# Kernel tuning notes

Measured on AMD Instinct MI355X. Metric: run time of the kernel, lower is better.

## Reference

```python
import jax, jax.numpy as jnp
import numpy as np

N, D_IN, D_OUT, L, R = 32768, 2048, 2048, 8, 16
LORA_ALPHA, LORA_RANK = 32.0, 16.0
SCALE = LORA_ALPHA / LORA_RANK  # applied because alpha != rank


def setup_inputs() -> dict:
    key = jax.random.key(0)
    ks = jax.random.split(key, 6)
    x = jax.random.normal(ks[0], (N, D_IN), dtype=jnp.float32)
    W = jax.random.normal(ks[1], (D_OUT, D_IN), dtype=jnp.float32) * 0.02
    b = jax.random.normal(ks[2], (D_OUT,), dtype=jnp.float32) * 0.02
    A_all = jax.random.normal(ks[3], (L, R, D_IN), dtype=jnp.float32) * 0.02
    B_all = jax.random.normal(ks[4], (L, D_OUT, R), dtype=jnp.float32) * 0.02
    # per-sample adapter index; -1 would mean "no LoRA" (handled by mask below)
    lora_idx = jax.random.randint(ks[5], (N,), 0, L, dtype=jnp.int32)
    return {"x": x, "W": W, "b": b, "A_all": A_all, "B_all": B_all, "lora_idx": lora_idx}


def reference(x, W, b, A_all, B_all, lora_idx):
    # Base linear: base_layer(x) -> x @ W.T + b
    base_out = x @ W.T + b  # [N, D_OUT]
    # Multi-LoRA: per-token adapter selection. Instead of Python grouping
    # (gather-matmul-scatter per group), compute the tiny down-projection for
    # all adapters and mask-select, then one fused up-projection.
    u = jnp.einsum('nd,lrd->nlr', x, A_all)  # [N, L, R] (small: r=16)
    Lnum = A_all.shape[0]
    sel = (lora_idx[:, None] == jnp.arange(Lnum, dtype=lora_idx.dtype)[None, :]) \
          & (lora_idx >= 0)[:, None]  # [N, L] one-hot, zero row if idx < 0
    u = u * sel[:, :, None].astype(u.dtype) * jnp.asarray(SCALE, u.dtype)
    # delta[n] = scale * (x[n] @ A[idx_n].T) @ B[idx_n].T, zeros elsewhere
    delta = jnp.einsum('nlr,lor->no', u, B_all)  # [N, D_OUT]
    return base_out + delta
```

## Files before the change

### kernel.cpp

```cpp
#include <hip/hip_runtime.h>
#include <stdint.h>

#define N_TOK 32768
#define DIN   2048
#define DOUT  2048
#define LAD   8
#define RRK   16
#define KCAT  2176
#define SCALE 2.0f

typedef __attribute__((ext_vector_type(8))) short bf16x8;
typedef __attribute__((ext_vector_type(4))) float f32x4;

__device__ __forceinline__ unsigned short f2bf(float f) {
    union { float f; unsigned u; } c; c.f = f;
    return (unsigned short)((c.u + 0x7FFFu + ((c.u >> 16) & 1u)) >> 16);
}

__device__ __forceinline__ uint4 pack8(float4 a, float4 b) {
    union { unsigned short s[8]; uint4 v; } u;
    u.s[0] = f2bf(a.x); u.s[1] = f2bf(a.y); u.s[2] = f2bf(a.z); u.s[3] = f2bf(a.w);
    u.s[4] = f2bf(b.x); u.s[5] = f2bf(b.y); u.s[6] = f2bf(b.z); u.s[7] = f2bf(b.w);
    return u.v;
}

__device__ __forceinline__ void async16(const void* g, void* l) {
    __builtin_amdgcn_global_load_lds(
        (const __attribute__((address_space(1))) void*)g,
        (__attribute__((address_space(3))) void*)l, 16, 0, 0);
}

__global__ __launch_bounds__(256) void prep_w(const float* __restrict__ W,
                                              const float* __restrict__ A_all,
                                              const float* __restrict__ B_all,
                                              unsigned short* __restrict__ wcat,
                                              unsigned short* __restrict__ acat) {
    const int NW = DOUT * DIN / 8;
    const int NB = DOUT * LAD;
    const int NA = LAD * RRK * DIN / 8;
    int tid = blockIdx.x * 256 + threadIdx.x;
    if (tid < NW) {
        int e = tid * 8;
        int o = e / DIN, k = e % DIN;
        float4 f0 = *(const float4*)(W + e);
        float4 f1 = *(const float4*)(W + e + 4);
        *(uint4*)(wcat + (size_t)o * KCAT + k) = pack8(f0, f1);
    } else if (tid < NW + NB) {
        int t = tid - NW;
        int o = t >> 3, l = t & 7;
        const float* src = B_all + ((size_t)l * DOUT + o) * RRK;
        float4 f0 = *(const float4*)(src + 0);
        float4 f1 = *(const float4*)(src + 4);
        float4 f2 = *(const float4*)(src + 8);
        float4 f3 = *(const float4*)(src + 12);
        unsigned short* dst = wcat + (size_t)o * KCAT + DIN + l * RRK;
        *(uint4*)(dst + 0) = pack8(f0, f1);
        *(uint4*)(dst + 8) = pack8(f2, f3);
    } else if (tid < NW + NB + NA) {
        int e = (tid - NW - NB) * 8;
        float4 f0 = *(const float4*)(A_all + e);
        float4 f1 = *(const float4*)(A_all + e + 4);
        *(uint4*)(acat + e) = pack8(f0, f1);
    }
}

__global__ __launch_bounds__(256) void conv_x(const float* __restrict__ x,
                                              unsigned short* __restrict__ xcat) {
    size_t e = ((size_t)blockIdx.x * 256 + threadIdx.x) * 8;
    int n = (int)(e / DIN), k = (int)(e % DIN);
    float4 f0 = *(const float4*)(x + e);
    float4 f1 = *(const float4*)(x + e + 4);
    *(uint4*)(xcat + (size_t)n * KCAT + k) = pack8(f0, f1);
}

__global__ __launch_bounds__(256) void u_gemm(const unsigned short* __restrict__ xcat,
                                              const unsigned short* __restrict__ acat,
                                              const int* __restrict__ lidx,
                                              unsigned short* __restrict__ xcat_w) {
    __shared__ short As[128 * 32];
    __shared__ short Bs[128 * 32];
    const int tid = threadIdx.x;
    const int lane = tid & 63, wv = tid >> 6;
    const int wm = wv >> 1, wn = wv & 1;
    const int quad = lane >> 4, lm = lane & 15;
    const int row0 = blockIdx.x * 128;
    const int sg = (lane & 3) ^ ((lane >> 3) & 3);
    const int swg = quad ^ ((lm >> 1) & 3);

    f32x4 acc[4][4];
    f32x4 zero = {0.f, 0.f, 0.f, 0.f};
#pragma unroll
    for (int i = 0; i < 4; ++i)
#pragma unroll
        for (int j = 0; j < 4; ++j) acc[i][j] = zero;

    for (int kt = 0; kt < DIN / 32; ++kt) {
        const unsigned short* ga = xcat + (size_t)row0 * KCAT + kt * 32;
        const unsigned short* gb = acat + kt * 32;
        __syncthreads();
#pragma unroll
        for (int it = 0; it < 2; ++it) {
            int cw = it * 4 + wv;
            int r = (cw * 64 + lane) >> 2;
            async16(ga + (size_t)r * KCAT + sg * 8, (void*)(As + cw * 512));
            async16(gb + (size_t)r * DIN + sg * 8, (void*)(Bs + cw * 512));
        }
        __syncthreads();
        bf16x8 a[4], b[4];
#pragma unroll
        for (int mi = 0; mi < 4; ++mi)
            a[mi] = *(const bf16x8*)&As[(wm * 64 + mi * 16 + lm) * 32 + swg * 8];
#pragma unroll
        for (int ni = 0; ni < 4; ++ni)
            b[ni] = *(const bf16x8*)&Bs[(wn * 64 + ni * 16 + lm) * 32 + swg * 8];
#pragma unroll
        for (int mi = 0; mi < 4; ++mi)
#pragma unroll
            for (int ni = 0; ni < 4; ++ni)
                acc[mi][ni] = __builtin_amdgcn_mfma_f32_16x16x32_bf16(a[mi], b[ni], acc[mi][ni], 0, 0, 0);
    }

#pragma unroll
    for (int mi = 0; mi < 4; ++mi) {
#pragma unroll
        for (int e = 0; e < 4; ++e) {
            int t = row0 + wm * 64 + mi * 16 + quad * 4 + e;
            int l = lidx[t];
#pragma unroll
            for (int ni = 0; ni < 4; ++ni) {
                int j = wn * 64 + ni * 16 + lm;
                float v = ((j >> 4) == l) ? acc[mi][ni][e] * SCALE : 0.0f;
                xcat_w[(size_t)t * KCAT + DIN + j] = f2bf(v);
            }
        }
    }
}

#define BK2  64
#define NKT2 (KCAT / BK2)
#define NIT  (NKT2 / 2)

#define VMC4() asm volatile("s_waitcnt vmcnt(4)" ::: "memory")
#define VMC0() asm volatile("s_waitcnt vmcnt(0)" ::: "memory")
#define LGK8() asm volatile("s_waitcnt lgkmcnt(8)" ::: "memory")
#define LGK0() asm volatile("s_waitcnt lgkmcnt(0)" ::: "memory")
#define BARR() __builtin_amdgcn_s_barrier()
#define SBR()  __builtin_amdgcn_sched_barrier(0)
#define PRIO1() __builtin_amdgcn_s_setprio(1)
#define PRIO0() __builtin_amdgcn_s_setprio(0)

#define RD_A(D, QM)                                                            \
    _Pragma("unroll") for (int mi = 0; mi < 4; ++mi)                           \
    _Pragma("unroll") for (int ks = 0; ks < 2; ++ks) {                         \
        const int rl = ((QM) * 4 + mi) * 16 + lm;                              \
        const int ob = (rl * 128 + ks * 64 + quad * 16) ^ ((lm & 7) << 4);     \
        aF[mi * 2 + ks] = *(const bf16x8*)((const char*)&lds[D][wm][0] + ob);  \
    }

#define RD_B(D, QN, BF)                                                        \
    _Pragma("unroll") for (int ni = 0; ni < 2; ++ni)                           \
    _Pragma("unroll") for (int ks = 0; ks < 2; ++ks) {                         \
        const int rl = (wn & 1) * 64 + ((QN) * 2 + ni) * 16 + lm;              \
        const int ob = (rl * 128 + ks * 64 + quad * 16) ^ ((lm & 7) << 4);     \
        BF[ni * 2 + ks] =                                                      \
            *(const bf16x8*)((const char*)&lds[D][2 + (wn >> 1)][0] + ob);     \
    }

#define MFMA16(QM, QN, BF)                                                     \
    _Pragma("unroll") for (int mi = 0; mi < 4; ++mi)                           \
    _Pragma("unroll") for (int ni = 0; ni < 2; ++ni)                           \
    _Pragma("unroll") for (int ks = 0; ks < 2; ++ks)                           \
        acc[(QM) * 4 + mi][(QN) * 2 + ni] =                                    \
            __builtin_amdgcn_mfma_f32_16x16x32_bf16(                           \
                aF[mi * 2 + ks], BF[ni * 2 + ks],                              \
                acc[(QM) * 4 + mi][(QN) * 2 + ni], 0, 0, 0);

__global__ __launch_bounds__(512, 2) void gemm_main(const unsigned short* __restrict__ xcat,
                                                    const unsigned short* __restrict__ wcat,
                                                    const float* __restrict__ bias,
                                                    float* __restrict__ out) {
    __shared__ short lds[2][4][8192];
    const int tid = threadIdx.x;
    const int lane = tid & 63, wv = tid >> 6;
    const int wm = wv >> 2, wn = wv & 3;
    const int quad = lane >> 4, lm = lane & 15;

    const int orig = blockIdx.x;
    const int swz = (orig & 7) * ((int)gridDim.x >> 3) + (orig >> 3);
    const int col0 = (swz & 7) * 256;
    const int row0 = (swz >> 3) * 256;

    const int rbase = wv * 8 + (lane >> 3);
    const int csrc = ((((lane & 7) * 16) ^ (((lane >> 3) & 7) << 4)) >> 1);

    auto stage = [&](int buf, int part, int gk) {
        const int half = part & 1;
        const unsigned short* g = (part < 2)
            ? xcat + (size_t)(row0 + half * 128) * KCAT
            : wcat + (size_t)(col0 + half * 128) * KCAT;
        short* dbase = &lds[buf][part][0] + wv * 512;
#pragma unroll
        for (int j = 0; j < 2; ++j)
            async16(g + (size_t)(j * 64 + rbase) * KCAT + gk * 64 + csrc,
                    (void*)(dbase + j * 4096));
    };

    f32x4 acc[8][4];
    f32x4 zero = {0.f, 0.f, 0.f, 0.f};
#pragma unroll
    for (int i = 0; i < 8; ++i)
#pragma unroll
        for (int j = 0; j < 4; ++j) acc[i][j] = zero;

    bf16x8 aF[8];
    bf16x8 bF0[4], bF1[4];

    stage(0, 0, 0); stage(0, 1, 0); stage(0, 2, 0); stage(0, 3, 0);
    stage(1, 2, 1); stage(1, 3, 1);
    VMC4();
    BARR();

    for (int it = 0; it < NIT - 1; ++it) {
        RD_A(0, 0) RD_B(0, 0, bF0)
        stage(1, 0, 2 * it + 1); LGK8();
        BARR(); LGK0(); SBR(); PRIO1(); MFMA16(0, 0, bF0) PRIO0(); BARR();
        RD_B(0, 1, bF1)
        stage(1, 1, 2 * it + 1);
        BARR(); LGK0(); SBR(); PRIO1(); MFMA16(0, 1, bF1) PRIO0(); BARR();
        RD_A(0, 1)
        stage(0, 2, 2 * it + 2);
        BARR(); LGK0(); SBR(); PRIO1(); MFMA16(1, 1, bF1) PRIO0(); BARR();
        stage(0, 3, 2 * it + 2);
        BARR(); PRIO1(); MFMA16(1, 0, bF0) PRIO0(); VMC4(); BARR();

        RD_A(1, 0) RD_B(1, 0, bF0)
        stage(0, 0, 2 * it + 2); LGK8();
        BARR(); LGK0(); SBR(); PRIO1(); MFMA16(0, 0, bF0) PRIO0(); BARR();
        RD_B(1, 1, bF1)
        stage(0, 1, 2 * it + 2);
        BARR(); LGK0(); SBR(); PRIO1(); MFMA16(0, 1, bF1) PRIO0(); BARR();
        RD_A(1, 1)
        stage(1, 2, 2 * it + 3);
        BARR(); LGK0(); SBR(); PRIO1(); MFMA16(1, 1, bF1) PRIO0(); BARR();
        stage(1, 3, 2 * it + 3);
        BARR(); PRIO1(); MFMA16(1, 0, bF0) PRIO0(); VMC4(); BARR();
    }

    RD_A(0, 0) RD_B(0, 0, bF0)
    stage(1, 0, 2 * (NIT - 1) + 1); LGK8();
    BARR(); LGK0(); SBR(); PRIO1(); MFMA16(0, 0, bF0) PRIO0(); BARR();
    RD_B(0, 1, bF1)
    stage(1, 1, 2 * (NIT - 1) + 1);
    BARR(); LGK0(); SBR(); PRIO1(); MFMA16(0, 1, bF1) PRIO0(); BARR();
    RD_A(0, 1)
    BARR(); LGK0(); SBR(); PRIO1(); MFMA16(1, 1, bF1) PRIO0(); BARR();
    BARR(); PRIO1(); MFMA16(1, 0, bF0) PRIO0(); VMC0(); BARR();
    RD_A(1, 0) RD_B(1, 0, bF0)
    BARR(); LGK0(); SBR(); PRIO1(); MFMA16(0, 0, bF0) PRIO0(); BARR();
    RD_B(1, 1, bF1)
    BARR(); LGK0(); SBR(); PRIO1(); MFMA16(0, 1, bF1) PRIO0(); BARR();
    RD_A(1, 1)
    BARR(); LGK0(); SBR(); PRIO1(); MFMA16(1, 1, bF1) PRIO0(); BARR();
    PRIO1(); MFMA16(1, 0, bF0) PRIO0();

#pragma unroll
    for (int ni = 0; ni < 4; ++ni) {
        int col = col0 + wn * 64 + ni * 16 + lm;
        float bv = bias[col];
#pragma unroll
        for (int mi = 0; mi < 8; ++mi) {
            int rbase2 = row0 + wm * 128 + mi * 16 + quad * 4;
#pragma unroll
            for (int e = 0; e < 4; ++e)
                out[(size_t)(rbase2 + e) * DOUT + col] = acc[mi][ni][e] + bv;
        }
    }
}

extern "C" void kernel_launch(void* const* d_in, const int* in_sizes, int n_in,
                              void* d_out, int out_size, void* d_ws, size_t ws_size,
                              hipStream_t stream) {
    const float* x     = (const float*)d_in[0];
    const float* W     = (const float*)d_in[1];
    const float* bias  = (const float*)d_in[2];
    const float* A_all = (const float*)d_in[3];
    const float* B_all = (const float*)d_in[4];
    const int*   lidx  = (const int*)d_in[5];
    float* out = (float*)d_out;

    char* ws = (char*)d_ws;
    unsigned short* xcat = (unsigned short*)ws;
    unsigned short* wcat = (unsigned short*)(ws + (size_t)N_TOK * KCAT * 2);
    unsigned short* acat = (unsigned short*)(ws + (size_t)N_TOK * KCAT * 2
                                                + (size_t)DOUT * KCAT * 2);

    prep_w<<<2240, 256, 0, stream>>>(W, A_all, B_all, wcat, acat);
    conv_x<<<(N_TOK * (DIN / 8)) / 256, 256, 0, stream>>>(x, xcat);
    u_gemm<<<N_TOK / 128, 256, 0, stream>>>(xcat, acat, lidx, xcat);
    gemm_main<<<dim3((N_TOK / 256) * (DOUT / 256)), 512, 0, stream>>>(xcat, wcat, bias, out);
}
```

Measured before the change: 788.9 us.

## Fuse x bf16 conversion into LoRA down-projection GEMM and hoist B fragment reads

Merges the fp32-to-bf16 conversion of x with the LoRA down-projection: a new kernel reads fp32 x directly, converts it in registers, writes the bf16 copy into the concatenated buffer, and feeds MFMAs with it, with a double-buffered adapter tile. This removes one full pass that re-reads the bf16 x copy from memory and drops a kernel launch. Separately, the main GEMM moves the first B-fragment LDS read ahead of the preceding barrier so it overlaps the tail of the previous MFMA phase. The fused kernel gives each wave a single 16-row strip with 16 fragment registers, so register pressure and occupancy may differ from before.

```diff
diff --git a/kernel.cpp b/kernel.cpp
--- a/kernel.cpp
+++ b/kernel.cpp
@@ -22,6 +22,12 @@
     u.s[0] = f2bf(a.x); u.s[1] = f2bf(a.y); u.s[2] = f2bf(a.z); u.s[3] = f2bf(a.w);
     u.s[4] = f2bf(b.x); u.s[5] = f2bf(b.y); u.s[6] = f2bf(b.z); u.s[7] = f2bf(b.w);
     return u.v;
+}
+
+__device__ __forceinline__ bf16x8 cvt8(float4 a, float4 b) {
+    union { uint4 v; bf16x8 h; } u;
+    u.v = pack8(a, b);
+    return u.h;
 }
 
 __device__ __forceinline__ void async16(const void* g, void* l) {
@@ -64,74 +70,85 @@
     }
 }
 
-__global__ __launch_bounds__(256) void conv_x(const float* __restrict__ x,
-                                              unsigned short* __restrict__ xcat) {
-    size_t e = ((size_t)blockIdx.x * 256 + threadIdx.x) * 8;
-    int n = (int)(e / DIN), k = (int)(e % DIN);
-    float4 f0 = *(const float4*)(x + e);
-    float4 f1 = *(const float4*)(x + e + 4);
-    *(uint4*)(xcat + (size_t)n * KCAT + k) = pack8(f0, f1);
-}
-
-__global__ __launch_bounds__(256) void u_gemm(const unsigned short* __restrict__ xcat,
-                                              const unsigned short* __restrict__ acat,
-                                              const int* __restrict__ lidx,
-                                              unsigned short* __restrict__ xcat_w) {
-    __shared__ short As[128 * 32];
-    __shared__ short Bs[128 * 32];
+__global__ __launch_bounds__(512, 2) void xu_gemm(const float* __restrict__ x,
+                                                  const unsigned short* __restrict__ acat,
+                                                  const int* __restrict__ lidx,
+                                                  unsigned short* __restrict__ xcat) {
+    __shared__ short Bs[2][8192];
     const int tid = threadIdx.x;
     const int lane = tid & 63, wv = tid >> 6;
-    const int wm = wv >> 1, wn = wv & 1;
     const int quad = lane >> 4, lm = lane & 15;
     const int row0 = blockIdx.x * 128;
-    const int sg = (lane & 3) ^ ((lane >> 3) & 3);
-    const int swg = quad ^ ((lm >> 1) & 3);
-
-    f32x4 acc[4][4];
+
+    const int rbase = wv * 8 + (lane >> 3);
+    const int csrc = ((((lane & 7) * 16) ^ (((lane >> 3) & 7) << 4)) >> 1);
+
+    auto stageB = [&](int kt, int buf) {
+        short* dbase = &Bs[buf][0] + wv * 512;
+#pragma unroll
+        for (int j = 0; j < 2; ++j)
+            async16(acat + (size_t)(j * 64 + rbase) * DIN + kt * 64 + csrc,
+                    (void*)(dbase + j * 4096));
+    };
+
+    const int myrow = row0 + wv * 16 + lm;
+    const float* gx = x + (size_t)myrow * DIN + quad * 8;
+    unsigned short* gxc = xcat + (size_t)myrow * KCAT + quad * 8;
+
+    f32x4 acc[8];
     f32x4 zero = {0.f, 0.f, 0.f, 0.f};
 #pragma unroll
-    for (int i = 0; i < 4; ++i)
-#pragma unroll
-        for (int j = 0; j < 4; ++j) acc[i][j] = zero;
-
-    for (int kt = 0; kt < DIN / 32; ++kt) {
-        const unsigned short* ga = xcat + (size_t)row0 * KCAT + kt * 32;
-        const unsigned short* gb = acat + kt * 32;
-        __syncthreads();
-#pragma unroll
-        for (int it = 0; it < 2; ++it) {
-            int cw = it * 4 + wv;
-            int r = (cw * 64 + lane) >> 2;
-            async16(ga + (size_t)r * KCAT + sg * 8, (void*)(As + cw * 512));
-            async16(gb + (size_t)r * DIN + sg * 8, (void*)(Bs + cw * 512));
+    for (int i = 0; i < 8; ++i) acc[i] = zero;
+
+    stageB(0, 0);
+    stageB(1, 1);
+    asm volatile("s_waitcnt vmcnt(2)" ::: "memory");
+    __builtin_amdgcn_s_barrier();
+
+    for (int t = 0; t < 32; ++t) {
+        const int buf = t & 1;
+        bf16x8 bF[16];
+#pragma unroll
+        for (int nj = 0; nj < 8; ++nj)
+#pragma unroll
+            for (int ks = 0; ks < 2; ++ks) {
+                const int rl = nj * 16 + lm;
+                const int ob = (rl * 128 + ks * 64 + quad * 16) ^ ((lm & 7) << 4);
+                bF[nj * 2 + ks] = *(const bf16x8*)((const char*)&Bs[buf][0] + ob);
+            }
+        float4 xa0 = *(const float4*)(gx + t * 64 + 0);
+        float4 xa1 = *(const float4*)(gx + t * 64 + 4);
+        float4 xb0 = *(const float4*)(gx + t * 64 + 32);
+        float4 xb1 = *(const float4*)(gx + t * 64 + 36);
+        asm volatile("s_waitcnt lgkmcnt(0)" ::: "memory");
+        __builtin_amdgcn_s_barrier();
+        stageB(t + 2 < 32 ? t + 2 : 31, buf);
+        if (t < 31)
+            asm volatile("s_waitcnt vmcnt(2)" ::: "memory");
+        else
+            asm volatile("s_waitcnt vmcnt(0)" ::: "memory");
+        bf16x8 aF0 = cvt8(xa0, xa1);
+        bf16x8 aF1 = cvt8(xb0, xb1);
+        union { bf16x8 h; uint4 v; } s0, s1;
+        s0.h = aF0; s1.h = aF1;
+        *(uint4*)(gxc + t * 64 + 0)  = s0.v;
+        *(uint4*)(gxc + t * 64 + 32) = s1.v;
+#pragma unroll
+        for (int nj = 0; nj < 8; ++nj) {
+            acc[nj] = __builtin_amdgcn_mfma_f32_16x16x32_bf16(aF0, bF[nj * 2 + 0], acc[nj], 0, 0, 0);
+            acc[nj] = __builtin_amdgcn_mfma_f32_16x16x32_bf16(aF1, bF[nj * 2 + 1], acc[nj], 0, 0, 0);
         }
-        __syncthreads();
-        bf16x8 a[4], b[4];
-#pragma unroll
-        for (int mi = 0; mi < 4; ++mi)
-            a[mi] = *(const bf16x8*)&As[(wm * 64 + mi * 16 + lm) * 32 + swg * 8];
-#pragma unroll
-        for (int ni = 0; ni < 4; ++ni)
-            b[ni] = *(const bf16x8*)&Bs[(wn * 64 + ni * 16 + lm) * 32 + swg * 8];
-#pragma unroll
-        for (int mi = 0; mi < 4; ++mi)
-#pragma unroll
-            for (int ni = 0; ni < 4; ++ni)
-                acc[mi][ni] = __builtin_amdgcn_mfma_f32_16x16x32_bf16(a[mi], b[ni], acc[mi][ni], 0, 0, 0);
-    }
-
-#pragma unroll
-    for (int mi = 0; mi < 4; ++mi) {
-#pragma unroll
-        for (int e = 0; e < 4; ++e) {
-            int t = row0 + wm * 64 + mi * 16 + quad * 4 + e;
-            int l = lidx[t];
-#pragma unroll
-            for (int ni = 0; ni < 4; ++ni) {
-                int j = wn * 64 + ni * 16 + lm;
-                float v = ((j >> 4) == l) ? acc[mi][ni][e] * SCALE : 0.0f;
-                xcat_w[(size_t)t * KCAT + DIN + j] = f2bf(v);
-            }
+        __builtin_amdgcn_s_barrier();
+    }
+
+#pragma unroll
+    for (int e = 0; e < 4; ++e) {
+        int t = row0 + wv * 16 + quad * 4 + e;
+        int l = lidx[t];
+#pragma unroll
+        for (int nj = 0; nj < 8; ++nj) {
+            float v = (nj == l) ? acc[nj][e] * SCALE : 0.0f;
+            xcat[(size_t)t * KCAT + DIN + nj * 16 + lm] = f2bf(v);
         }
     }
 }
@@ -219,9 +236,10 @@
     stage(1, 2, 1); stage(1, 3, 1);
     VMC4();
     BARR();
+    RD_B(0, 0, bF0)
 
     for (int it = 0; it < NIT - 1; ++it) {
-        RD_A(0, 0) RD_B(0, 0, bF0)
+        RD_A(0, 0)
         stage(1, 0, 2 * it + 1); LGK8();
         BARR(); LGK0(); SBR(); PRIO1(); MFMA16(0, 0, bF0) PRIO0(); BARR();
         RD_B(0, 1, bF1)
@@ -231,9 +249,11 @@
         stage(0, 2, 2 * it + 2);
         BARR(); LGK0(); SBR(); PRIO1(); MFMA16(1, 1, bF1) PRIO0(); BARR();
         stage(0, 3, 2 * it + 2);
-        BARR(); PRIO1(); MFMA16(1, 0, bF0) PRIO0(); VMC4(); BARR();
-
-        RD_A(1, 0) RD_B(1, 0, bF0)
+        BARR(); PRIO1(); MFMA16(1, 0, bF0) PRIO0(); VMC4();
+        RD_B(1, 0, bF0)
+        BARR();
+
+        RD_A(1, 0)
         stage(0, 0, 2 * it + 2); LGK8();
         BARR(); LGK0(); SBR(); PRIO1(); MFMA16(0, 0, bF0) PRIO0(); BARR();
         RD_B(1, 1, bF1)
@@ -243,10 +263,12 @@
         stage(1, 2, 2 * it + 3);
         BARR(); LGK0(); SBR(); PRIO1(); MFMA16(1, 1, bF1) PRIO0(); BARR();
         stage(1, 3, 2 * it + 3);
-        BARR(); PRIO1(); MFMA16(1, 0, bF0) PRIO0(); VMC4(); BARR();
-    }
-
-    RD_A(0, 0) RD_B(0, 0, bF0)
+        BARR(); PRIO1(); MFMA16(1, 0, bF0) PRIO0(); VMC4();
+        RD_B(0, 0, bF0)
+        BARR();
+    }
+
+    RD_A(0, 0)
     stage(1, 0, 2 * (NIT - 1) + 1); LGK8();
     BARR(); LGK0(); SBR(); PRIO1(); MFMA16(0, 0, bF0) PRIO0(); BARR();
     RD_B(0, 1, bF1)
@@ -254,8 +276,10 @@
     BARR(); LGK0(); SBR(); PRIO1(); MFMA16(0, 1, bF1) PRIO0(); BARR();
     RD_A(0, 1)
     BARR(); LGK0(); SBR(); PRIO1(); MFMA16(1, 1, bF1) PRIO0(); BARR();
-    BARR(); PRIO1(); MFMA16(1, 0, bF0) PRIO0(); VMC0(); BARR();
-    RD_A(1, 0) RD_B(1, 0, bF0)
+    BARR(); PRIO1(); MFMA16(1, 0, bF0) PRIO0(); VMC0();
+    RD_B(1, 0, bF0)
+    BARR();
+    RD_A(1, 0)
     BARR(); LGK0(); SBR(); PRIO1(); MFMA16(0, 0, bF0) PRIO0(); BARR();
     RD_B(1, 1, bF1)
     BARR(); LGK0(); SBR(); PRIO1(); MFMA16(0, 1, bF1) PRIO0(); BARR();
@@ -295,7 +319,6 @@
                                                 + (size_t)DOUT * KCAT * 2);
 
     prep_w<<<2240, 256, 0, stream>>>(W, A_all, B_all, wcat, acat);
-    conv_x<<<(N_TOK * (DIN / 8)) / 256, 256, 0, stream>>>(x, xcat);
-    u_gemm<<<N_TOK / 128, 256, 0, stream>>>(xcat, acat, lidx, xcat);
+    xu_gemm<<<N_TOK / 128, 512, 0, stream>>>(x, acat, lidx, xcat);
     gemm_main<<<dim3((N_TOK / 256) * (DOUT / 256)), 512, 0, stream>>>(xcat, wcat, bias, out);
 }
```

Measured after the change: 772.7 us. 2.1% less time.
